# Kernel tuning notes

Hardware: AMD Instinct MI355X
Metric: run time of the kernel (lower is better)

## Reference

```python
import jax, jax.numpy as jnp
import numpy as np

N, IN_DIM, HEADS, C = 50000, 78, 10, 78
HC = HEADS * C          # 780
E = 400000
B = 256
NEG_SLOPE = 0.2


def setup_inputs() -> dict:
    key = jax.random.key(0)
    ks = jax.random.split(key, 10)
    x = jax.random.normal(ks[0], (N, IN_DIM), dtype=jnp.float32)
    edge_index = jax.random.randint(ks[1], (2, E), 0, N, dtype=jnp.int64)
    batch = jnp.sort(jax.random.randint(ks[2], (N,), 0, B, dtype=jnp.int64))
    s = 1.0 / np.sqrt(IN_DIM)
    W_l = jax.random.uniform(ks[3], (IN_DIM, HC), jnp.float32, -s, s)
    W_r = jax.random.uniform(ks[4], (IN_DIM, HC), jnp.float32, -s, s)
    att = jax.random.uniform(ks[5], (HEADS, C), jnp.float32, -1.0 / np.sqrt(C), 1.0 / np.sqrt(C))
    bias1 = jnp.zeros((HC,), jnp.float32)
    s2 = 1.0 / np.sqrt(HC)
    W_gcn = jax.random.uniform(ks[6], (HC, HC), jnp.float32, -s2, s2)
    bias_gcn = jnp.zeros((HC,), jnp.float32)
    return {"x": x, "edge_index": edge_index, "batch": batch,
            "W_l": W_l, "W_r": W_r, "att": att, "bias1": bias1,
            "W_gcn": W_gcn, "bias_gcn": bias_gcn}


def _add_self_loops(edge_index, n):
    loops = jnp.arange(n, dtype=edge_index.dtype)
    return jnp.concatenate([edge_index, jnp.stack([loops, loops])], axis=1)


def _gatv2(x, edge_index, W_l, W_r, att, bias):
    ei = _add_self_loops(edge_index, x.shape[0])
    src, dst = ei[0], ei[1]                      # message j -> i
    xl = (x @ W_l).reshape(-1, HEADS, C)         # [N,H,C]
    xr = (x @ W_r).reshape(-1, HEADS, C)
    e = xl[src] + xr[dst]                        # [E',H,C]
    e = jnp.where(e > 0, e, NEG_SLOPE * e)       # leaky_relu
    score = jnp.einsum('ehc,hc->eh', e, att)     # [E',H]
    # segment softmax over destination node
    m = jax.ops.segment_max(score, dst, num_segments=x.shape[0])
    ex = jnp.exp(score - m[dst])
    denom = jax.ops.segment_sum(ex, dst, num_segments=x.shape[0])
    alpha = ex / denom[dst]                      # [E',H]
    out = jax.ops.segment_sum(alpha[:, :, None] * xl[src], dst,
                              num_segments=x.shape[0])  # [N,H,C]
    return out.reshape(-1, HC) + bias


def _gcn(x, edge_index, W, bias):
    n = x.shape[0]
    ei = _add_self_loops(edge_index, n)
    src, dst = ei[0], ei[1]
    deg = jax.ops.segment_sum(jnp.ones_like(src, dtype=x.dtype), dst, num_segments=n)
    dinv = jax.lax.rsqrt(jnp.maximum(deg, 1e-12))
    norm = dinv[src] * dinv[dst]                 # [E']
    h = x @ W
    out = jax.ops.segment_sum(norm[:, None] * h[src], dst, num_segments=n)
    return out + bias


def reference(x, edge_index, batch, W_l, W_r, att, bias1, W_gcn, bias_gcn):
    # eval mode: dropout = identity
    h = jax.nn.elu(_gatv2(x, edge_index, W_l, W_r, att, bias1))
    h = _gcn(h, edge_index, W_gcn, bias_gcn)
    h = jax.nn.relu(h)
    gmax = jax.ops.segment_max(h, batch, num_segments=B)
    gmax = jnp.where(jnp.isfinite(gmax), gmax, 0.0)
    cnt = jax.ops.segment_sum(jnp.ones((h.shape[0], 1), h.dtype), batch, num_segments=B)
    gmean = jax.ops.segment_sum(h, batch, num_segments=B) / jnp.maximum(cnt, 1.0)
    return jnp.concatenate([gmax, gmean], axis=1)   # [B, 2*HC]
```

## Files before the change

### kernel.cpp

```cpp
#include <hip/hip_runtime.h>
#include <hip/hip_bf16.h>
#include <math.h>

#define NNODES   50000
#define INDIM    78
#define NHEADS   10
#define CDIM     78
#define HCDIM    780
#define NEDGES   400000
#define NBATCH   256
#define ETOT     (NEDGES + NNODES)
#define NEG_SLOPE 0.2f

#define BM 128
#define BN 128
#define BK 64
#define KPAD 832
#define NPAD 896
#define LDT 68

#define KP1 128
#define NP1 1664

typedef __attribute__((ext_vector_type(8))) short bf16x8_t;
typedef __attribute__((ext_vector_type(4))) float f32x4_t;
typedef __attribute__((ext_vector_type(2))) float v2f;

__device__ __forceinline__ float bf2f(unsigned short u) {
    union { unsigned int i; float f; } v; v.i = ((unsigned int)u) << 16; return v.f;
}
__device__ __forceinline__ unsigned short f2bf(float f) {
    __hip_bfloat16 h = __float2bfloat16(f);
    return *reinterpret_cast<unsigned short*>(&h);
}
__device__ __forceinline__ v2f cvt2(unsigned int u) {
    union { unsigned int i; float f; } lo, hi;
    lo.i = u << 16;
    hi.i = u & 0xFFFF0000u;
    v2f r; r.x = lo.f; r.y = hi.f; return r;
}
__device__ __forceinline__ v2f vabs2(v2f t) {
    union { v2f f; unsigned long long u; } x; x.f = t;
    x.u &= 0x7FFFFFFF7FFFFFFFull; return x.f;
}
__device__ __forceinline__ float dpp_red16(float x) {
    int y;
    y = __builtin_amdgcn_update_dpp(0, __float_as_int(x), 0xB1, 0xF, 0xF, true);
    x += __int_as_float(y);
    y = __builtin_amdgcn_update_dpp(0, __float_as_int(x), 0x4E, 0xF, 0xF, true);
    x += __int_as_float(y);
    y = __builtin_amdgcn_update_dpp(0, __float_as_int(x), 0x141, 0xF, 0xF, true);
    x += __int_as_float(y);
    y = __builtin_amdgcn_update_dpp(0, __float_as_int(x), 0x140, 0xF, 0xF, true);
    x += __int_as_float(y);
    return x;
}

__device__ __forceinline__ void async_ld16(const unsigned short* g, unsigned short* l) {
    __builtin_amdgcn_global_load_lds(
        (const __attribute__((address_space(1))) void*)g,
        (__attribute__((address_space(3))) void*)l, 16, 0, 0);
}

__global__ void zero_kernel(float* __restrict__ outp, int nf, int* __restrict__ deg, int ni) {
    int i = blockIdx.x * blockDim.x + threadIdx.x;
    if (i < nf) outp[i] = 0.f;
    if (i < ni) deg[i] = 0;
}

__global__ void count_kernel(const int* __restrict__ ei, int* __restrict__ deg) {
    int e = blockIdx.x * blockDim.x + threadIdx.x;
    if (e >= ETOT) return;
    int d = (e < NEDGES) ? ei[NEDGES + e] : (e - NEDGES);
    atomicAdd(&deg[d], 1);
}

__global__ void scan1_kernel(const int* __restrict__ deg, int* __restrict__ rowp,
                             int* __restrict__ bsum) {
    __shared__ int s[256];
    int t = threadIdx.x, b = blockIdx.x;
    int i = b * 256 + t;
    int v = (i < NNODES) ? deg[i] : 0;
    s[t] = v;
    __syncthreads();
    #pragma unroll
    for (int off = 1; off < 256; off <<= 1) {
        int y = (t >= off) ? s[t - off] : 0;
        __syncthreads();
        s[t] += y;
        __syncthreads();
    }
    int incl = s[t];
    if (i < NNODES) rowp[i] = incl - v;
    if (t == 255) bsum[b] = incl;
}

__global__ void scan2_kernel(int* __restrict__ bsum, int* __restrict__ rowp, int nblk,
                             const int* __restrict__ batch, int* __restrict__ bst) {
    __shared__ int s[256];
    int t = threadIdx.x;
    int v = 0;
    if (t < 256) { v = (t < nblk) ? bsum[t] : 0; s[t] = v; }
    __syncthreads();
    #pragma unroll
    for (int off = 1; off < 256; off <<= 1) {
        int y = (t < 256 && t >= off) ? s[t - off] : 0;
        __syncthreads();
        if (t < 256) s[t] += y;
        __syncthreads();
    }
    if (t < 256) {
        int incl = s[t];
        if (t < nblk) bsum[t] = incl - v;
        if (t == 255) rowp[NNODES] = incl;
    } else {
        int b = t - 256;
        int lo = 0, hi = NNODES;
        while (lo < hi) { int mid = (lo + hi) >> 1; if (batch[mid] < b) lo = mid + 1; else hi = mid; }
        bst[b] = lo;
        if (t == 511) bst[NBATCH] = NNODES;
    }
}

__global__ void scan3_kernel(int* __restrict__ rowp, const int* __restrict__ bsum,
                             int* __restrict__ curs, const int* __restrict__ deg,
                             float* __restrict__ dinv) {
    int i = blockIdx.x * 256 + threadIdx.x;
    if (i >= NNODES) return;
    int r = rowp[i] + bsum[i >> 8];
    rowp[i] = r;
    curs[i] = r;
    dinv[i] = rsqrtf((float)deg[i]);
}

__global__ void fill_kernel(const int* __restrict__ ei,
                            int* __restrict__ cursor, int* __restrict__ col) {
    int e = blockIdx.x * blockDim.x + threadIdx.x;
    if (e >= ETOT) return;
    int s, d;
    if (e < NEDGES) { s = ei[e]; d = ei[NEDGES + e]; }
    else            { s = d = e - NEDGES; }
    int pos = atomicAdd(&cursor[d], 1);
    col[pos] = s;
}

__global__ void wprep_kernel(const float* __restrict__ Wl, const float* __restrict__ Wr,
                             unsigned short* __restrict__ Wc) {
    int idx = blockIdx.x * 256 + threadIdx.x;
    if (idx >= NP1 * KP1) return;
    int n = idx >> 7, k = idx & 127;
    float v = 0.f;
    if (k < INDIM) {
        if (n < HCDIM)            v = Wl[(size_t)k * HCDIM + n];
        else if (n < 2 * HCDIM)   v = Wr[(size_t)k * HCDIM + (n - HCDIM)];
    }
    Wc[idx] = f2bf(v);
}

__global__ __launch_bounds__(256) void gemm1_kernel(
        const float* __restrict__ x, const unsigned short* __restrict__ Wc,
        unsigned short* __restrict__ xl, unsigned short* __restrict__ xr, int M) {
    __shared__ unsigned short As[4 * 4096];
    __shared__ unsigned short Bs[4 * 4096];
    int t = threadIdx.x;
    int lane = t & 63, w = t >> 6;
    int bm = blockIdx.x * 128;

    for (int idx = t; idx < 128 * 128; idx += 256) {
        int row = idx >> 7, k = idx & 127;
        int kc = k >> 5, ch = (k >> 3) & 3, e = k & 7;
        int gr = bm + row;
        float v = (gr < M && k < INDIM) ? x[(size_t)gr * INDIM + k] : 0.f;
        As[kc * 4096 + row * 32 + (((ch + (row >> 1)) & 3) * 8) + e] = f2bf(v);
    }

    int lrow = lane >> 2;
    int gch = ((lane & 3) - (lane >> 3)) & 3;
    int m16 = lane & 15, q = lane >> 4;
    int wr = (w >> 1) * 64, wcc = (w & 1) * 64;

    for (int nb = 0; nb < 13; nb++) {
        __syncthreads();
        #pragma unroll
        for (int kc = 0; kc < 4; kc++) {
            const unsigned short* gb = Wc + ((size_t)(nb * 128 + 32 * w + lrow)) * KP1
                                          + kc * 32 + gch * 8;
            unsigned short* lb = Bs + kc * 4096 + (32 * w) * 32;
            async_ld16(gb, lb);
            async_ld16(gb + 16 * KP1, lb + 16 * 32);
        }
        __syncthreads();

        f32x4_t acc[4][4];
        #pragma unroll
        for (int i = 0; i < 4; i++)
            #pragma unroll
            for (int j = 0; j < 4; j++)
                acc[i][j] = (f32x4_t)(0.f);

        #pragma unroll
        for (int kc = 0; kc < 4; kc++) {
            bf16x8_t af[4], bf[4];
            #pragma unroll
            for (int i = 0; i < 4; i++) {
                int row = wr + i * 16 + m16;
                af[i] = *(const bf16x8_t*)&As[kc * 4096 + row * 32 + (((q + (row >> 1)) & 3) * 8)];
            }
            #pragma unroll
            for (int j = 0; j < 4; j++) {
                int row = wcc + j * 16 + m16;
                bf[j] = *(const bf16x8_t*)&Bs[kc * 4096 + row * 32 + (((q + (row >> 1)) & 3) * 8)];
            }
            #pragma unroll
            for (int i = 0; i < 4; i++)
                #pragma unroll
                for (int j = 0; j < 4; j++)
                    acc[i][j] = __builtin_amdgcn_mfma_f32_16x16x32_bf16(af[i], bf[j], acc[i][j], 0, 0, 0);
        }

        #pragma unroll
        for (int j = 0; j < 4; j++) {
            int ng = nb * 128 + wcc + j * 16 + m16;
            if (ng >= 2 * HCDIM) continue;
            unsigned short* dst = (ng < HCDIM) ? (xl + ng) : (xr + (ng - HCDIM));
            #pragma unroll
            for (int i = 0; i < 4; i++) {
                #pragma unroll
                for (int rr = 0; rr < 4; rr++) {
                    int row = bm + wr + i * 16 + q * 4 + rr;
                    if (row < M) dst[(size_t)row * HCDIM] = f2bf(acc[i][j][rr]);
                }
            }
        }
    }
}

__device__ __forceinline__ void gat_body(
        const unsigned int* __restrict__ xp, int cl, bool lo7, bool live,
        v2f r0, v2f r1, v2f r2,
        v2f a60, v2f a61, v2f a62, v2f a40, v2f a41, v2f a42,
        float& l, v2f& acc0, v2f& acc1, v2f& acc2) {
    unsigned int u0 = xp[cl];
    unsigned int u1 = xp[cl + 16];
    unsigned int u2 = lo7 ? xp[cl + 32] : 0u;
    v2f v0 = cvt2(u0), v1 = cvt2(u1), v2v = cvt2(u2);
    v2f t0 = v0 + r0, t1 = v1 + r1, t2 = v2v + r2;
    v2f s2 = t0 * a60 + vabs2(t0) * a40;
    s2 += t1 * a61 + vabs2(t1) * a41;
    s2 += t2 * a62 + vabs2(t2) * a42;
    float part = dpp_red16(s2.x + s2.y);
    float p = __builtin_amdgcn_exp2f(part);
    p = live ? p : 0.f;
    l += p;
    acc0 += p * v0; acc1 += p * v1; acc2 += p * v2v;
}

__global__ __launch_bounds__(256) void gat_kernel(
        const unsigned short* __restrict__ xl, const unsigned short* xr,
        const int* __restrict__ row_ptr, const int* __restrict__ col,
        const float* __restrict__ att, const float* __restrict__ bias1,
        unsigned short* h_out) {
    int wid = blockIdx.x * 4 + (threadIdx.x >> 6);
    int pair = wid / 5;
    int slot = wid - 5 * pair;
    if (pair >= NNODES / 2) return;
    int lane = threadIdx.x & 63;
    int g = lane >> 4, cl = lane & 15;
    bool lo7 = cl < 7;
    bool strad = (slot == 4);
    int node, head;
    if (!strad) { node = 2 * pair + (slot >> 1); head = ((slot & 1) << 2) + g; }
    else        { node = 2 * pair + (g >> 1);    head = 8 + (g & 1); }
    int hcl = head * (CDIM / 2);
    const unsigned int* xlu = (const unsigned int*)xl;
    const unsigned int* xru = (const unsigned int*)xr;

    const float L6 = 0.6f * 1.4426950408889634f;
    const float L4 = 0.4f * 1.4426950408889634f;
    const float2* ap = (const float2*)(att + head * CDIM);
    float2 f0 = ap[cl], f1 = ap[cl + 16];
    float2 f2 = lo7 ? ap[cl + 32] : make_float2(0.f, 0.f);
    v2f a60, a61, a62, a40, a41, a42;
    a60.x = f0.x * L6; a60.y = f0.y * L6;
    a61.x = f1.x * L6; a61.y = f1.y * L6;
    a62.x = f2.x * L6; a62.y = f2.y * L6;
    a40.x = f0.x * L4; a40.y = f0.y * L4;
    a41.x = f1.x * L4; a41.y = f1.y * L4;
    a42.x = f2.x * L4; a42.y = f2.y * L4;

    const unsigned int* xrp = xru + (size_t)node * (HCDIM / 2) + hcl;
    v2f r0 = cvt2(xrp[cl]);
    v2f r1 = cvt2(xrp[cl + 16]);
    v2f r2 = lo7 ? cvt2(xrp[cl + 32]) : (v2f)(0.f);

    float l = 0.f;
    v2f acc0 = (v2f)(0.f), acc1 = (v2f)(0.f), acc2 = (v2f)(0.f);

    if (!strad) {
        int e0 = row_ptr[node], e1 = row_ptr[node + 1];
        int e = e0;
        for (; e + 2 <= e1; e += 2) {
            int ja = __builtin_amdgcn_readfirstlane(col[e]);
            int jb = __builtin_amdgcn_readfirstlane(col[e + 1]);
            gat_body(xlu + (size_t)ja * (HCDIM / 2) + hcl, cl, lo7, true,
                     r0, r1, r2, a60, a61, a62, a40, a41, a42, l, acc0, acc1, acc2);
            gat_body(xlu + (size_t)jb * (HCDIM / 2) + hcl, cl, lo7, true,
                     r0, r1, r2, a60, a61, a62, a40, a41, a42, l, acc0, acc1, acc2);
        }
        if (e < e1) {
            int j = __builtin_amdgcn_readfirstlane(col[e]);
            gat_body(xlu + (size_t)j * (HCDIM / 2) + hcl, cl, lo7, true,
                     r0, r1, r2, a60, a61, a62, a40, a41, a42, l, acc0, acc1, acc2);
        }
    } else {
        int re0 = row_ptr[node], re1 = row_ptr[node + 1];
        int deg = re1 - re0;
        int dA = __builtin_amdgcn_readlane(deg, 0);
        int dB = __builtin_amdgcn_readlane(deg, 32);
        int iters = dA > dB ? dA : dB;
        for (int i = 0; i < iters; i++) {
            bool live = i < deg;
            int ec = re0 + (live ? i : deg - 1);
            int j = col[ec];
            gat_body(xlu + (size_t)j * (HCDIM / 2) + hcl, cl, lo7, live,
                     r0, r1, r2, a60, a61, a62, a40, a41, a42, l, acc0, acc1, acc2);
        }
    }

    float inv = 1.f / l;
    size_t rbase = (size_t)node * HCDIM + head * CDIM;
    const float2* bp = (const float2*)(bias1 + head * CDIM);
    unsigned int* op = (unsigned int*)(h_out + rbase);
    #pragma unroll
    for (int k = 0; k < 3; k++) {
        if (k == 2 && !lo7) break;
        v2f a = (k == 0) ? acc0 : (k == 1) ? acc1 : acc2;
        float2 bb = bp[cl + 16 * k];
        float x0 = a.x * inv + bb.x;
        float x1 = a.y * inv + bb.y;
        x0 = x0 > 0.f ? x0 : (__expf(x0) - 1.f);
        x1 = x1 > 0.f ? x1 : (__expf(x1) - 1.f);
        unsigned int o = (unsigned int)f2bf(x0) | ((unsigned int)f2bf(x1) << 16);
        op[cl + 16 * k] = o;
    }
}

__global__ __launch_bounds__(256) void gcn_agg_kernel(
        const unsigned short* __restrict__ h, const int* __restrict__ row_ptr,
        const int* __restrict__ col, const float* __restrict__ dinv,
        unsigned short* __restrict__ agg) {
    int node = blockIdx.x * 4 + (threadIdx.x >> 6);
    if (node >= NNODES) return;
    int ln = threadIdx.x & 63;
    bool hasC = ln < 3;
    float accA[8] = {}, accB[4] = {}, accC[4] = {};
    int e0 = row_ptr[node], e1 = row_ptr[node + 1];
    int e = e0;
    int jn = (e < e1) ? col[e] : 0;
    for (; e < e1; ) {
        int j = __builtin_amdgcn_readfirstlane(jn);
        ++e;
        jn = (e < e1) ? col[e] : 0;
        float s = dinv[j];
        const unsigned short* hr = h + (size_t)j * HCDIM;
        bf16x8_t u = *(const bf16x8_t*)(hr + 8 * ln);
        ushort4 v4 = *(const ushort4*)(hr + 512 + 4 * ln);
        ushort4 w4 = hasC ? *(const ushort4*)(hr + 768 + 4 * ln) : make_ushort4(0, 0, 0, 0);
        #pragma unroll
        for (int k = 0; k < 8; k++) accA[k] = fmaf(s, bf2f((unsigned short)u[k]), accA[k]);
        accB[0] = fmaf(s, bf2f(v4.x), accB[0]);
        accB[1] = fmaf(s, bf2f(v4.y), accB[1]);
        accB[2] = fmaf(s, bf2f(v4.z), accB[2]);
        accB[3] = fmaf(s, bf2f(v4.w), accB[3]);
        accC[0] = fmaf(s, bf2f(w4.x), accC[0]);
        accC[1] = fmaf(s, bf2f(w4.y), accC[1]);
        accC[2] = fmaf(s, bf2f(w4.z), accC[2]);
        accC[3] = fmaf(s, bf2f(w4.w), accC[3]);
    }
    float di = dinv[node];
    unsigned short* ar = agg + (size_t)node * HCDIM;
    ushort4 o1, o2, ob;
    o1.x = f2bf(accA[0] * di); o1.y = f2bf(accA[1] * di);
    o1.z = f2bf(accA[2] * di); o1.w = f2bf(accA[3] * di);
    o2.x = f2bf(accA[4] * di); o2.y = f2bf(accA[5] * di);
    o2.z = f2bf(accA[6] * di); o2.w = f2bf(accA[7] * di);
    ob.x = f2bf(accB[0] * di); ob.y = f2bf(accB[1] * di);
    ob.z = f2bf(accB[2] * di); ob.w = f2bf(accB[3] * di);
    *(ushort4*)(ar + 8 * ln) = o1;
    *(ushort4*)(ar + 8 * ln + 4) = o2;
    *(ushort4*)(ar + 512 + 4 * ln) = ob;
    if (hasC) {
        ushort4 oc;
        oc.x = f2bf(accC[0] * di); oc.y = f2bf(accC[1] * di);
        oc.z = f2bf(accC[2] * di); oc.w = f2bf(accC[3] * di);
        *(ushort4*)(ar + 768 + 4 * ln) = oc;
    }
}

__global__ void btprep_kernel(const float* __restrict__ W, unsigned short* __restrict__ BT) {
    int idx = blockIdx.x * 256 + threadIdx.x;
    if (idx >= NPAD * KPAD) return;
    int n = idx / KPAD, k = idx - n * KPAD;
    float v = (n < HCDIM && k < HCDIM) ? W[(size_t)k * HCDIM + n] : 0.f;
    BT[idx] = f2bf(v);
}

__global__ __launch_bounds__(256) void gemm2_pool_kernel(
        const unsigned short* __restrict__ A, const unsigned short* __restrict__ BT,
        const float* __restrict__ bias, const int* __restrict__ batch,
        float* __restrict__ out, int M) {
    int f = blockIdx.x;
    int xcd = f & 7, inner = f >> 3;
    int bq = inner / 7, colt = inner - 7 * bq;
    int band = 8 * bq + xcd;
    if (band >= (M + BM - 1) / BM) return;
    int bm = band * BM, bn = colt * BN;

    __shared__ unsigned short smem[2 * 128 * 64];
    unsigned short* As = smem;
    unsigned short* Bs = smem + 128 * 64;
    __shared__ int bsh[BM];

    int t = threadIdx.x;
    int lane = t & 63, w = t >> 6;

    if (t < BM) {
        int row = bm + t;
        bsh[t] = (row < M) ? batch[row] : -1;
    }

    int m16 = lane & 15, q = lane >> 4;
    int wr = (w >> 1) * 64, wc = (w & 1) * 64;

    int lrow8 = lane >> 3;
    int c8 = lane & 7;
    int gch = (c8 - lrow8) & 7;
    const unsigned short* gA = A  + (size_t)(bm + 32 * w + lrow8) * HCDIM + gch * 8;
    const unsigned short* gB = BT + (size_t)(bn + 32 * w + lrow8) * KPAD  + gch * 8;
    unsigned short* lA = As + (32 * w) * 64;
    unsigned short* lB = Bs + (32 * w) * 64;

    f32x4_t acc[4][4];
    #pragma unroll
    for (int i = 0; i < 4; i++)
        #pragma unroll
        for (int j = 0; j < 4; j++)
            acc[i][j] = (f32x4_t)(0.f);

    for (int k0 = 0; k0 < KPAD; k0 += BK) {
        __syncthreads();
        #pragma unroll
        for (int ib = 0; ib < 4; ib++) {
            async_ld16(gA + (size_t)(8 * ib) * HCDIM + k0, lA + (8 * ib) * 64);
            async_ld16(gB + (size_t)(8 * ib) * KPAD  + k0, lB + (8 * ib) * 64);
        }
        __syncthreads();

        #pragma unroll
        for (int half = 0; half < 2; half++) {
            bf16x8_t af[4], bf[4];
            #pragma unroll
            for (int i = 0; i < 4; i++) {
                int row = wr + i * 16 + m16;
                af[i] = *(const bf16x8_t*)&As[row * 64 + ((4 * half + q + row) & 7) * 8];
            }
            #pragma unroll
            for (int j = 0; j < 4; j++) {
                int row = wc + j * 16 + m16;
                bf[j] = *(const bf16x8_t*)&Bs[row * 64 + ((4 * half + q + row) & 7) * 8];
            }
            #pragma unroll
            for (int i = 0; i < 4; i++)
                #pragma unroll
                for (int j = 0; j < 4; j++)
                    acc[i][j] = __builtin_amdgcn_mfma_f32_16x16x32_bf16(af[i], bf[j], acc[i][j], 0, 0, 0);
        }
    }

    float bvj[4];
    #pragma unroll
    for (int j = 0; j < 4; j++) {
        int gcc = bn + wc + j * 16 + m16;
        bvj[j] = (gcc < HCDIM) ? bias[gcc] : 0.f;
    }

    #pragma unroll
    for (int p = 0; p < 2; p++) {
        __syncthreads();
        if ((w >> 1) == p) {
            #pragma unroll
            for (int i = 0; i < 4; i++) {
                #pragma unroll
                for (int j = 0; j < 4; j++) {
                    int colc = wc + j * 16 + m16;
                    ushort4 o;
                    float v0 = acc[i][j][0] + bvj[j];
                    float v1 = acc[i][j][1] + bvj[j];
                    float v2 = acc[i][j][2] + bvj[j];
                    float v3 = acc[i][j][3] + bvj[j];
                    o.x = f2bf(v0 > 0.f ? v0 : 0.f);
                    o.y = f2bf(v1 > 0.f ? v1 : 0.f);
                    o.z = f2bf(v2 > 0.f ? v2 : 0.f);
                    o.w = f2bf(v3 > 0.f ? v3 : 0.f);
                    *(ushort4*)&smem[colc * LDT + i * 16 + q * 4] = o;
                }
            }
        }
        __syncthreads();
        int colp = t & 127;
        int rb = (t >> 7) * 32;
        int gc = bn + colp;
        if (gc < HCDIM) {
            int cur = -1; float mx = 0.f, sm = 0.f;
            bool done = false;
            for (int rr = rb; rr < rb + 32 && !done; rr += 4) {
                ushort4 u = *(const ushort4*)&smem[colp * LDT + rr];
                unsigned short us[4] = {u.x, u.y, u.z, u.w};
                #pragma unroll
                for (int s2 = 0; s2 < 4; s2++) {
                    int b = bsh[64 * p + rr + s2];
                    if (b < 0) { done = true; break; }
                    float v = bf2f(us[s2]);
                    if (b != cur) {
                        if (cur >= 0) {
                            atomicMax((int*)(out + (size_t)cur * (2 * HCDIM) + gc), __float_as_int(mx));
                            atomicAdd(out + (size_t)cur * (2 * HCDIM) + HCDIM + gc, sm);
                        }
                        cur = b; mx = v; sm = v;
                    } else { mx = fmaxf(mx, v); sm += v; }
                }
            }
            if (cur >= 0) {
                atomicMax((int*)(out + (size_t)cur * (2 * HCDIM) + gc), __float_as_int(mx));
                atomicAdd(out + (size_t)cur * (2 * HCDIM) + HCDIM + gc, sm);
            }
        }
    }
}

__global__ void finalize_kernel(float* __restrict__ out, const int* __restrict__ bst) {
    int i = blockIdx.x * blockDim.x + threadIdx.x;
    if (i >= NBATCH * HCDIM) return;
    int b = i / HCDIM, c = i - b * HCDIM;
    int cnt = bst[b + 1] - bst[b];
    out[(size_t)b * (2 * HCDIM) + HCDIM + c] /= (float)(cnt > 0 ? cnt : 1);
}

extern "C" void kernel_launch(void* const* d_in, const int* in_sizes, int n_in,
                              void* d_out, int out_size, void* d_ws, size_t ws_size,
                              hipStream_t stream) {
    const float* x       = (const float*)d_in[0];
    const int*   ei      = (const int*)d_in[1];
    const int*   batch   = (const int*)d_in[2];
    const float* W_l     = (const float*)d_in[3];
    const float* W_r     = (const float*)d_in[4];
    const float* att     = (const float*)d_in[5];
    const float* bias1   = (const float*)d_in[6];
    const float* W_gcn   = (const float*)d_in[7];
    const float* bias_gcn= (const float*)d_in[8];
    float* out = (float*)d_out;

    char* w = (char*)d_ws;
    const size_t BIGH = (size_t)NNODES * HCDIM * sizeof(unsigned short);
    unsigned short* xl  = (unsigned short*)(w);
    unsigned short* xr  = (unsigned short*)(w + BIGH);
    unsigned short* agg = xl;
    unsigned short* BT  = xr;
    char* sm = w + 2 * BIGH;
    int*   rowp = (int*)(sm);                    sm += 50048 * 4;
    int*   col  = (int*)(sm);                    sm += 450048 * 4;
    float* dinv = (float*)(sm);                  sm += 50048 * 4;
    int*   bst  = (int*)(sm);                    sm += 512 * 4;
    int*   bsum = (int*)(sm);                    sm += 256 * 4;
    char* S = sm;                                sm += 426240;
    int*   deg  = (int*)(S);
    int*   curs = (int*)(S + 200192);
    unsigned short* Wc = (unsigned short*)(S);
    size_t needed = (size_t)(sm - (char*)d_ws);
    if (ws_size < needed) return;

    zero_kernel<<<(NBATCH * 2 * HCDIM + 255) / 256, 256, 0, stream>>>(
        out, NBATCH * 2 * HCDIM, deg, NNODES);

    {
        int eblocks = (ETOT + 255) / 256;
        int nblocks = (NNODES + 255) / 256;
        count_kernel<<<eblocks, 256, 0, stream>>>(ei, deg);
        scan1_kernel<<<nblocks, 256, 0, stream>>>(deg, rowp, bsum);
        scan2_kernel<<<1, 512, 0, stream>>>(bsum, rowp, nblocks, batch, bst);
        scan3_kernel<<<nblocks, 256, 0, stream>>>(rowp, bsum, curs, deg, dinv);
        fill_kernel<<<eblocks, 256, 0, stream>>>(ei, curs, col);
    }

    wprep_kernel<<<(NP1 * KP1 + 255) / 256, 256, 0, stream>>>(W_l, W_r, Wc);

    gemm1_kernel<<<(NNODES + 127) / 128, 256, 0, stream>>>(x, Wc, xl, xr, NNODES);

    {
        int waves = (NNODES / 2) * 5;
        int blocks = (waves + 3) / 4;
        gat_kernel<<<blocks, 256, 0, stream>>>(xl, xr, rowp, col, att, bias1, xr);
    }

    gcn_agg_kernel<<<(NNODES + 3) / 4, 256, 0, stream>>>(xr, rowp, col, dinv, agg);

    btprep_kernel<<<(NPAD * KPAD + 255) / 256, 256, 0, stream>>>(W_gcn, BT);

    {
        int nb = (NNODES + BM - 1) / BM;
        int gx = 8 * ((nb + 7) / 8) * 7;
        gemm2_pool_kernel<<<gx, 256, 0, stream>>>(agg, BT, bias_gcn, batch, out, NNODES);
    }

    finalize_kernel<<<(NBATCH * HCDIM + 255) / 256, 256, 0, stream>>>(out, bst);
}
```

Before: 649.6 us.

## Remap GAT attention to 8-lane head groups covering four nodes per five waves

The GAT aggregation kernel now gives each (node, head) pair 8 lanes instead of 16, so five waves cover four nodes and 40 head slots. The old split between uniform waves and a straddling wave goes away, and every wave runs a lockstep loop over the larger of the first and last node's degree, masking dead iterations. Leaky-relu now uses a max instead of the abs-based split, column loads use clamped unsigned byte offsets, and the reduction is one DPP step shorter. The intent is to halve the wave count and cut instruction overhead, at the cost of more per-lane registers and divergent masked iterations when the degrees of a wave's nodes differ.

```diff
diff --git a/kernel.cpp b/kernel.cpp
--- a/kernel.cpp
+++ b/kernel.cpp
@@ -39,19 +39,16 @@
     hi.i = u & 0xFFFF0000u;
     v2f r; r.x = lo.f; r.y = hi.f; return r;
 }
-__device__ __forceinline__ v2f vabs2(v2f t) {
-    union { v2f f; unsigned long long u; } x; x.f = t;
-    x.u &= 0x7FFFFFFF7FFFFFFFull; return x.f;
-}
-__device__ __forceinline__ float dpp_red16(float x) {
+__device__ __forceinline__ v2f vmax2(v2f a, v2f b) {
+    v2f r; r.x = fmaxf(a.x, b.x); r.y = fmaxf(a.y, b.y); return r;
+}
+__device__ __forceinline__ float dpp_red8(float x) {
     int y;
     y = __builtin_amdgcn_update_dpp(0, __float_as_int(x), 0xB1, 0xF, 0xF, true);
     x += __int_as_float(y);
     y = __builtin_amdgcn_update_dpp(0, __float_as_int(x), 0x4E, 0xF, 0xF, true);
     x += __int_as_float(y);
     y = __builtin_amdgcn_update_dpp(0, __float_as_int(x), 0x141, 0xF, 0xF, true);
-    x += __int_as_float(y);
-    y = __builtin_amdgcn_update_dpp(0, __float_as_int(x), 0x140, 0xF, 0xF, true);
     x += __int_as_float(y);
     return x;
 }
@@ -235,24 +232,34 @@
     }
 }
 
-__device__ __forceinline__ void gat_body(
-        const unsigned int* __restrict__ xp, int cl, bool lo7, bool live,
-        v2f r0, v2f r1, v2f r2,
-        v2f a60, v2f a61, v2f a62, v2f a40, v2f a41, v2f a42,
-        float& l, v2f& acc0, v2f& acc1, v2f& acc2) {
-    unsigned int u0 = xp[cl];
-    unsigned int u1 = xp[cl + 16];
-    unsigned int u2 = lo7 ? xp[cl + 32] : 0u;
-    v2f v0 = cvt2(u0), v1 = cvt2(u1), v2v = cvt2(u2);
-    v2f t0 = v0 + r0, t1 = v1 + r1, t2 = v2v + r2;
-    v2f s2 = t0 * a60 + vabs2(t0) * a40;
-    s2 += t1 * a61 + vabs2(t1) * a41;
-    s2 += t2 * a62 + vabs2(t2) * a42;
-    float part = dpp_red16(s2.x + s2.y);
-    float p = __builtin_amdgcn_exp2f(part);
-    p = live ? p : 0.f;
-    l += p;
-    acc0 += p * v0; acc1 += p * v1; acc2 += p * v2v;
+__device__ __forceinline__ void gat_body8(
+        const char* __restrict__ xlb, unsigned bo, bool lo7, bool live,
+        v2f r0, v2f r1, v2f r2, v2f r3, v2f r4,
+        v2f a0, v2f a1, v2f a2, v2f a3, v2f a4,
+        float& l, v2f& c0, v2f& c1, v2f& c2, v2f& c3, v2f& c4) {
+    const unsigned int* p = (const unsigned int*)(xlb + bo);
+    unsigned int u0 = p[0];
+    unsigned int u1 = p[8];
+    unsigned int u2 = p[16];
+    unsigned int u3 = p[24];
+    unsigned int u4 = lo7 ? p[32] : 0u;
+    v2f v0 = cvt2(u0), v1 = cvt2(u1), v2v = cvt2(u2), v3 = cvt2(u3), v4 = cvt2(u4);
+    v2f t0 = v0 + r0, t1 = v1 + r1, t2 = v2v + r2, t3 = v3 + r3, t4 = v4 + r4;
+    v2f m0 = vmax2(t0, t0 * 0.2f);
+    v2f m1 = vmax2(t1, t1 * 0.2f);
+    v2f m2 = vmax2(t2, t2 * 0.2f);
+    v2f m3 = vmax2(t3, t3 * 0.2f);
+    v2f m4 = vmax2(t4, t4 * 0.2f);
+    v2f s2 = m0 * a0;
+    s2 += m1 * a1;
+    s2 += m2 * a2;
+    s2 += m3 * a3;
+    s2 += m4 * a4;
+    float part = dpp_red8(s2.x + s2.y);
+    float pp = __builtin_amdgcn_exp2f(part);
+    pp = live ? pp : 0.f;
+    l += pp;
+    c0 += pp * v0; c1 += pp * v1; c2 += pp * v2v; c3 += pp * v3; c4 += pp * v4;
 }
 
 __global__ __launch_bounds__(256) void gat_kernel(
@@ -261,87 +268,78 @@
         const float* __restrict__ att, const float* __restrict__ bias1,
         unsigned short* h_out) {
     int wid = blockIdx.x * 4 + (threadIdx.x >> 6);
-    int pair = wid / 5;
-    int slot = wid - 5 * pair;
-    if (pair >= NNODES / 2) return;
+    int quad = wid / 5;
+    int wavein = wid - 5 * quad;
     int lane = threadIdx.x & 63;
-    int g = lane >> 4, cl = lane & 15;
-    bool lo7 = cl < 7;
-    bool strad = (slot == 4);
-    int node, head;
-    if (!strad) { node = 2 * pair + (slot >> 1); head = ((slot & 1) << 2) + g; }
-    else        { node = 2 * pair + (g >> 1);    head = 8 + (g & 1); }
-    int hcl = head * (CDIM / 2);
-    const unsigned int* xlu = (const unsigned int*)xl;
-    const unsigned int* xru = (const unsigned int*)xr;
-
-    const float L6 = 0.6f * 1.4426950408889634f;
-    const float L4 = 0.4f * 1.4426950408889634f;
+    int g = lane >> 3, gl = lane & 7;
+    int tau = 8 * wavein + g;
+    int nl = tau / 10;
+    int head = tau - 10 * nl;
+    int node = 4 * quad + nl;
+    bool lo7 = gl < 7;
+
+    const float L2E = 1.4426950408889634f;
     const float2* ap = (const float2*)(att + head * CDIM);
-    float2 f0 = ap[cl], f1 = ap[cl + 16];
-    float2 f2 = lo7 ? ap[cl + 32] : make_float2(0.f, 0.f);
-    v2f a60, a61, a62, a40, a41, a42;
-    a60.x = f0.x * L6; a60.y = f0.y * L6;
-    a61.x = f1.x * L6; a61.y = f1.y * L6;
-    a62.x = f2.x * L6; a62.y = f2.y * L6;
-    a40.x = f0.x * L4; a40.y = f0.y * L4;
-    a41.x = f1.x * L4; a41.y = f1.y * L4;
-    a42.x = f2.x * L4; a42.y = f2.y * L4;
-
-    const unsigned int* xrp = xru + (size_t)node * (HCDIM / 2) + hcl;
-    v2f r0 = cvt2(xrp[cl]);
-    v2f r1 = cvt2(xrp[cl + 16]);
-    v2f r2 = lo7 ? cvt2(xrp[cl + 32]) : (v2f)(0.f);
+    float2 A0 = ap[gl], A1 = ap[gl + 8], A2 = ap[gl + 16], A3 = ap[gl + 24];
+    float2 A4 = lo7 ? ap[gl + 32] : make_float2(0.f, 0.f);
+    v2f a0, a1, a2, a3, a4;
+    a0.x = A0.x * L2E; a0.y = A0.y * L2E;
+    a1.x = A1.x * L2E; a1.y = A1.y * L2E;
+    a2.x = A2.x * L2E; a2.y = A2.y * L2E;
+    a3.x = A3.x * L2E; a3.y = A3.y * L2E;
+    a4.x = A4.x * L2E; a4.y = A4.y * L2E;
+
+    unsigned doffb = (unsigned)(head * (CDIM * 2) + gl * 4);
+    const char* xlb = (const char*)xl;
+    const unsigned int* rp = (const unsigned int*)((const char*)xr
+                              + (unsigned)node * (unsigned)(HCDIM * 2) + doffb);
+    v2f r0 = cvt2(rp[0]);
+    v2f r1 = cvt2(rp[8]);
+    v2f r2 = cvt2(rp[16]);
+    v2f r3 = cvt2(rp[24]);
+    v2f r4 = lo7 ? cvt2(rp[32]) : (v2f)(0.f);
+
+    int e0 = row_ptr[node], e1 = row_ptr[node + 1];
+    int deg = e1 - e0;
+    int dF = __builtin_amdgcn_readlane(deg, 0);
+    int dL = __builtin_amdgcn_readlane(deg, 63);
+    int iters = dF > dL ? dF : dL;
 
     float l = 0.f;
-    v2f acc0 = (v2f)(0.f), acc1 = (v2f)(0.f), acc2 = (v2f)(0.f);
-
-    if (!strad) {
-        int e0 = row_ptr[node], e1 = row_ptr[node + 1];
-        int e = e0;
-        for (; e + 2 <= e1; e += 2) {
-            int ja = __builtin_amdgcn_readfirstlane(col[e]);
-            int jb = __builtin_amdgcn_readfirstlane(col[e + 1]);
-            gat_body(xlu + (size_t)ja * (HCDIM / 2) + hcl, cl, lo7, true,
-                     r0, r1, r2, a60, a61, a62, a40, a41, a42, l, acc0, acc1, acc2);
-            gat_body(xlu + (size_t)jb * (HCDIM / 2) + hcl, cl, lo7, true,
-                     r0, r1, r2, a60, a61, a62, a40, a41, a42, l, acc0, acc1, acc2);
-        }
-        if (e < e1) {
-            int j = __builtin_amdgcn_readfirstlane(col[e]);
-            gat_body(xlu + (size_t)j * (HCDIM / 2) + hcl, cl, lo7, true,
-                     r0, r1, r2, a60, a61, a62, a40, a41, a42, l, acc0, acc1, acc2);
-        }
-    } else {
-        int re0 = row_ptr[node], re1 = row_ptr[node + 1];
-        int deg = re1 - re0;
-        int dA = __builtin_amdgcn_readlane(deg, 0);
-        int dB = __builtin_amdgcn_readlane(deg, 32);
-        int iters = dA > dB ? dA : dB;
-        for (int i = 0; i < iters; i++) {
-            bool live = i < deg;
-            int ec = re0 + (live ? i : deg - 1);
-            int j = col[ec];
-            gat_body(xlu + (size_t)j * (HCDIM / 2) + hcl, cl, lo7, live,
-                     r0, r1, r2, a60, a61, a62, a40, a41, a42, l, acc0, acc1, acc2);
-        }
+    v2f c0 = (v2f)(0.f), c1 = (v2f)(0.f), c2 = (v2f)(0.f), c3 = (v2f)(0.f), c4 = (v2f)(0.f);
+
+    const char* colb = (const char*)col;
+    unsigned cbase = (unsigned)e0 * 4u;
+    unsigned cmax = (unsigned)(deg - 1) * 4u;
+    for (int i = 0; i < iters; i += 2) {
+        unsigned io = (unsigned)i * 4u;
+        unsigned q1 = io < cmax ? io : cmax;
+        unsigned io2 = io + 4u;
+        unsigned q2 = io2 < cmax ? io2 : cmax;
+        int j1 = *(const int*)(colb + (cbase + q1));
+        int j2 = *(const int*)(colb + (cbase + q2));
+        bool lv1 = i < deg;
+        bool lv2 = (i + 1) < deg;
+        gat_body8(xlb, (unsigned)j1 * (unsigned)(HCDIM * 2) + doffb, lo7, lv1,
+                  r0, r1, r2, r3, r4, a0, a1, a2, a3, a4, l, c0, c1, c2, c3, c4);
+        gat_body8(xlb, (unsigned)j2 * (unsigned)(HCDIM * 2) + doffb, lo7, lv2,
+                  r0, r1, r2, r3, r4, a0, a1, a2, a3, a4, l, c0, c1, c2, c3, c4);
     }
 
     float inv = 1.f / l;
-    size_t rbase = (size_t)node * HCDIM + head * CDIM;
     const float2* bp = (const float2*)(bias1 + head * CDIM);
-    unsigned int* op = (unsigned int*)(h_out + rbase);
+    unsigned int* op = (unsigned int*)((char*)h_out
+                        + (unsigned)node * (unsigned)(HCDIM * 2) + doffb);
     #pragma unroll
-    for (int k = 0; k < 3; k++) {
-        if (k == 2 && !lo7) break;
-        v2f a = (k == 0) ? acc0 : (k == 1) ? acc1 : acc2;
-        float2 bb = bp[cl + 16 * k];
-        float x0 = a.x * inv + bb.x;
-        float x1 = a.y * inv + bb.y;
+    for (int k = 0; k < 5; k++) {
+        if (k == 4 && !lo7) break;
+        v2f c = (k == 0) ? c0 : (k == 1) ? c1 : (k == 2) ? c2 : (k == 3) ? c3 : c4;
+        float2 bb = bp[gl + 8 * k];
+        float x0 = c.x * inv + bb.x;
+        float x1 = c.y * inv + bb.y;
         x0 = x0 > 0.f ? x0 : (__expf(x0) - 1.f);
         x1 = x1 > 0.f ? x1 : (__expf(x1) - 1.f);
-        unsigned int o = (unsigned int)f2bf(x0) | ((unsigned int)f2bf(x1) << 16);
-        op[cl + 16 * k] = o;
+        op[8 * k] = (unsigned int)f2bf(x0) | ((unsigned int)f2bf(x1) << 16);
     }
 }
 
@@ -597,8 +595,8 @@
     gemm1_kernel<<<(NNODES + 127) / 128, 256, 0, stream>>>(x, Wc, xl, xr, NNODES);
 
     {
-        int waves = (NNODES / 2) * 5;
-        int blocks = (waves + 3) / 4;
+        int waves = (NNODES / 4) * 5;
+        int blocks = waves / 4;
         gat_kernel<<<blocks, 256, 0, stream>>>(xl, xr, rowp, col, att, bias1, xr);
     }
 
```

Result: faster. 618.0 us (-4.9%).
